# Optimization experiments

Measured on AMD Instinct MI355X. Metric: run time of the kernel, lower is better.

Reference implementation:

```python
import jax, jax.numpy as jnp
import numpy as np

BSZ, SLEN, DIN = 4, 2048, 1024
EMB, HNO = 1024, 16
HSZ = EMB // HNO


def setup_inputs() -> dict:
    key = jax.random.key(0)
    ks = jax.random.split(key, 7)
    s = 1.0 / np.sqrt(DIN)
    return {
        "x": jax.random.normal(ks[0], (BSZ, SLEN, DIN), dtype=jnp.float32),
        "Wq": jax.random.uniform(ks[1], (EMB, DIN), jnp.float32, -s, s),
        "bq": jax.random.uniform(ks[2], (EMB,), jnp.float32, -s, s),
        "Wk": jax.random.uniform(ks[3], (EMB, DIN), jnp.float32, -s, s),
        "bk": jax.random.uniform(ks[4], (EMB,), jnp.float32, -s, s),
        "Wv": jax.random.uniform(ks[5], (EMB, DIN), jnp.float32, -s, s),
        "bv": jax.random.uniform(ks[6], (EMB,), jnp.float32, -s, s),
    }


def reference(x, Wq, bq, Wk, bk, Wv, bv):
    bsz, slen, _ = x.shape
    # QKV projections, split heads: [b, h, s, hd]
    def proj(W, b):
        y = jnp.einsum('bsd,ed->bse', x, W) + b
        return y.reshape(bsz, slen, HNO, HSZ).transpose(0, 2, 1, 3)
    q, k, v = proj(Wq, bq), proj(Wk, bk), proj(Wv, bv)
    # scaled causal attention scores [b, h, s, s]
    scores = jnp.einsum('bhqd,bhkd->bhqk', q, k) / jnp.sqrt(jnp.asarray(HSZ, x.dtype))
    causal = jnp.tril(jnp.ones((slen, slen), dtype=bool))
    scores = jnp.where(causal[None, None], scores, -jnp.inf)
    attn = jax.nn.softmax(scores, axis=-1)
    value = jnp.einsum('bhqk,bhkd->bhqd', attn, v)  # [b, h, s, hd]
    # faithful to source: swap (s, hd) THEN flatten to [b, s, emb]
    value = jnp.swapaxes(value, -2, -1).reshape(bsz, slen, -1)
    return value
```

## Files before the change

### kernel.cpp

```cpp
#include <hip/hip_runtime.h>


#define BSZ 4
#define SLEN 2048
#define DIN 1024
#define EMB 1024
#define HNO 16
#define HSZ 64

typedef unsigned short u16;
typedef __bf16 bf16x8_t __attribute__((ext_vector_type(8)));
typedef float f32x4_t __attribute__((ext_vector_type(4)));

__device__ __forceinline__ u16 f2bf(float f) {
    unsigned u = __float_as_uint(f);
    u += 0x7FFFu + ((u >> 16) & 1u);
    return (u16)(u >> 16);
}

__device__ __forceinline__ float exp2_fast(float x) {
    float r;
    asm("v_exp_f32 %0, %1" : "=v"(r) : "v"(x));
    return r;
}

__device__ __forceinline__ unsigned cvt_pk_bf16(float lo, float hi) {
    unsigned r;
    asm("v_cvt_pk_bf16_f32 %0, %1, %2" : "=v"(r) : "v"(lo), "v"(hi));
    return r;
}

__device__ __forceinline__ void gld16(void* lds, const void* g) {
    __builtin_amdgcn_global_load_lds(
        (const __attribute__((address_space(1))) void*)g,
        (__attribute__((address_space(3))) void*)lds, 16, 0, 0);
}

__global__ __launch_bounds__(256) void cvt_bf16_kernel(
    const float* __restrict__ x,  const float* __restrict__ wq,
    const float* __restrict__ wk, const float* __restrict__ wv,
    u16* __restrict__ xo, u16* __restrict__ wo)
{
    const int y = blockIdx.y;
    const float* src = (y == 0) ? x : (y == 1) ? wq : (y == 2) ? wk : wv;
    u16* dst = (y == 0) ? xo : wo + (size_t)(y - 1) * (EMB * DIN);
    const int n8 = (y == 0) ? (BSZ * SLEN * DIN / 8) : (EMB * DIN / 8);

    for (int i = blockIdx.x * 256 + threadIdx.x; i < n8; i += gridDim.x * 256) {
        float4 a = *reinterpret_cast<const float4*>(src + (size_t)i * 8);
        float4 b = *reinterpret_cast<const float4*>(src + (size_t)i * 8 + 4);
        union { u16 h[8]; uint4 u; } p;
        p.h[0] = f2bf(a.x); p.h[1] = f2bf(a.y); p.h[2] = f2bf(a.z); p.h[3] = f2bf(a.w);
        p.h[4] = f2bf(b.x); p.h[5] = f2bf(b.y); p.h[6] = f2bf(b.z); p.h[7] = f2bf(b.w);
        *reinterpret_cast<uint4*>(dst + (size_t)i * 8) = p.u;
    }
}

__global__ __launch_bounds__(256) void qkv_gemm_kernel(
    const u16* __restrict__ xb, const u16* __restrict__ wb,
    const float* __restrict__ bq, const float* __restrict__ bk,
    const float* __restrict__ bv,
    u16* __restrict__ qo, u16* __restrict__ ko, u16* __restrict__ vo)
{
    __shared__ __attribute__((aligned(16))) u16 As[128][32];
    __shared__ __attribute__((aligned(16))) u16 Bs[128][32];

    const int t    = threadIdx.x;
    const int wid  = t >> 6;
    const int lane = t & 63;
    const int g    = lane >> 4;
    const int r16  = lane & 15;

    const int m0  = blockIdx.x * 128;
    const int n0  = blockIdx.y * 128;
    const int mat = blockIdx.z;

    const u16*   W    = wb + (size_t)mat * (EMB * DIN);
    const float* bias = (mat == 0) ? bq : (mat == 1) ? bk : bv;
    u16*         outp = (mat == 0) ? qo : (mat == 1) ? ko : vo;
    const float  qs   = (mat == 0) ? 0.125f * 1.44269504f : 1.0f;

    const int wm = wid >> 1, wn = wid & 1;

    const int srow = lane >> 2;
    const int scol = (lane & 3) * 8;
    const u16* gA = xb + (size_t)(m0 + wid * 16 + srow) * DIN + scol;
    const u16* gB = W  + (size_t)(n0 + wid * 16 + srow) * DIN + scol;
    u16* lA0 = &As[wid * 16][0];
    u16* lA1 = &As[64 + wid * 16][0];
    u16* lB0 = &Bs[wid * 16][0];
    u16* lB1 = &Bs[64 + wid * 16][0];

    f32x4_t acc[4][4] = {};

    for (int k0 = 0; k0 < DIN; k0 += 32) {
        __syncthreads();
        gld16(lA0, gA + k0);
        gld16(lA1, gA + (size_t)64 * DIN + k0);
        gld16(lB0, gB + k0);
        gld16(lB1, gB + (size_t)64 * DIN + k0);
        __syncthreads();

        bf16x8_t af[4], bfv[4];
#pragma unroll
        for (int i = 0; i < 4; ++i)
            af[i] = *reinterpret_cast<const bf16x8_t*>(&As[wm * 64 + i * 16 + r16][g * 8]);
#pragma unroll
        for (int j = 0; j < 4; ++j)
            bfv[j] = *reinterpret_cast<const bf16x8_t*>(&Bs[wn * 64 + j * 16 + r16][g * 8]);
#pragma unroll
        for (int i = 0; i < 4; ++i)
#pragma unroll
            for (int j = 0; j < 4; ++j)
                acc[i][j] = __builtin_amdgcn_mfma_f32_16x16x32_bf16(af[i], bfv[j], acc[i][j], 0, 0, 0);
    }

#pragma unroll
    for (int j = 0; j < 4; ++j) {
        int e = n0 + wn * 64 + j * 16 + r16;
        float bv_ = bias[e];
        int h = e >> 6, d = e & 63;
#pragma unroll
        for (int i = 0; i < 4; ++i) {
#pragma unroll
            for (int r = 0; r < 4; ++r) {
                int m = m0 + wm * 64 + i * 16 + g * 4 + r;
                int b = m >> 11, s = m & 2047;
                float val = (acc[i][j][r] + bv_) * qs;
                outp[(((size_t)(b * HNO + h)) * SLEN + s) * HSZ + d] = f2bf(val);
            }
        }
    }
}

__global__ __launch_bounds__(512, 6) void attn_kernel(
    const u16* __restrict__ qb, const u16* __restrict__ kb,
    const u16* __restrict__ vb, float* __restrict__ out)
{
    __shared__ __attribute__((aligned(16))) u16 Ks[64][64];
    __shared__ __attribute__((aligned(16))) u16 Vt[64][72];
    __shared__ __attribute__((aligned(16))) u16 P2[8][16][72];

    const int t    = threadIdx.x;
    const int wid  = t >> 6;
    const int lane = t & 63;
    const int g    = lane >> 4;
    const int r16  = lane & 15;

    const int w   = blockIdx.x;
    const int idx = w >> 3;
    const int bh  = (w & 7) * 8 + (idx & 7);
    const int qt  = 15 - (idx >> 3);
    const int q0  = qt * 128;
    const size_t base = (size_t)bh * (SLEN * HSZ);

    const int qi = q0 + wid * 16 + r16;
    bf16x8_t qf0 = *reinterpret_cast<const bf16x8_t*>(&qb[base + (size_t)qi * HSZ + g * 8]);
    bf16x8_t qf1 = *reinterpret_cast<const bf16x8_t*>(&qb[base + (size_t)qi * HSZ + 32 + g * 8]);

    const int krl   = lane >> 3;
    const int kchunk = ((lane & 7) ^ krl) * 8;
    const int krow_g = wid * 8 + krl;
    u16* kdst = &Ks[wid * 8][0];

    const int va  = t & 31;
    const int vc4 = (t >> 5) * 4;

    const int ksl = ((g ^ (r16 & 7)) * 8);

    f32x4_t o[4] = {};
    float mrow = -1e30f, lrow = 0.f;

    const int ntiles = 2 * qt + 2;
    const int qw0 = q0 + wid * 16;
    const int qmax_wave = qw0 + 15;

    uint2 v0 = *reinterpret_cast<const uint2*>(&vb[base + (size_t)(2 * va) * HSZ + vc4]);
    uint2 v1 = *reinterpret_cast<const uint2*>(&vb[base + (size_t)(2 * va + 1) * HSZ + vc4]);

    for (int kt = 0; kt < ntiles; ++kt) {
        const int kv0 = kt * 64;
        __syncthreads();
        gld16(kdst, &kb[base + (size_t)(kv0 + krow_g) * HSZ + kchunk]);
        {
            const unsigned* pa = reinterpret_cast<const unsigned*>(&v0);
            const unsigned* pb = reinterpret_cast<const unsigned*>(&v1);
#pragma unroll
            for (int j2 = 0; j2 < 2; ++j2) {
                unsigned lo = __builtin_amdgcn_perm(pb[j2], pa[j2], 0x05040100u);
                unsigned hi = __builtin_amdgcn_perm(pb[j2], pa[j2], 0x07060302u);
                *reinterpret_cast<unsigned*>(&Vt[vc4 + 2 * j2][2 * va])     = lo;
                *reinterpret_cast<unsigned*>(&Vt[vc4 + 2 * j2 + 1][2 * va]) = hi;
            }
        }
        __syncthreads();

        if (kt + 1 < ntiles) {
            const size_t nb = base + (size_t)(kv0 + 64) * HSZ;
            v0 = *reinterpret_cast<const uint2*>(&vb[nb + (size_t)(2 * va) * HSZ + vc4]);
            v1 = *reinterpret_cast<const uint2*>(&vb[nb + (size_t)(2 * va + 1) * HSZ + vc4]);
        }

        if (kv0 > qmax_wave) continue;

        f32x4_t c_[4];
        __builtin_amdgcn_s_setprio(1);
#pragma unroll
        for (int m = 0; m < 4; ++m) {
            bf16x8_t a0 = *reinterpret_cast<const bf16x8_t*>(&Ks[m * 16 + r16][ksl]);
            bf16x8_t a1 = *reinterpret_cast<const bf16x8_t*>(&Ks[m * 16 + r16][ksl ^ 32]);
            f32x4_t cc = {};
            cc = __builtin_amdgcn_mfma_f32_16x16x32_bf16(a0, qf0, cc, 0, 0, 0);
            cc = __builtin_amdgcn_mfma_f32_16x16x32_bf16(a1, qf1, cc, 0, 0, 0);
            c_[m] = cc;
        }
        __builtin_amdgcn_s_setprio(0);

        float s[16];
        if (kv0 + 63 > qw0) {
#pragma unroll
            for (int m = 0; m < 4; ++m)
#pragma unroll
                for (int r = 0; r < 4; ++r) {
                    int kj = kv0 + m * 16 + g * 4 + r;
                    s[m * 4 + r] = (kj <= qi) ? c_[m][r] : -1e30f;
                }
        } else {
#pragma unroll
            for (int m = 0; m < 4; ++m)
#pragma unroll
                for (int r = 0; r < 4; ++r)
                    s[m * 4 + r] = c_[m][r];
        }
        float x0 = fmaxf(s[0], s[1]),   x1 = fmaxf(s[2], s[3]);
        float x2 = fmaxf(s[4], s[5]),   x3 = fmaxf(s[6], s[7]);
        float x4 = fmaxf(s[8], s[9]),   x5 = fmaxf(s[10], s[11]);
        float x6 = fmaxf(s[12], s[13]), x7 = fmaxf(s[14], s[15]);
        x0 = fmaxf(x0, x1); x2 = fmaxf(x2, x3); x4 = fmaxf(x4, x5); x6 = fmaxf(x6, x7);
        float tmax = fmaxf(fmaxf(x0, x2), fmaxf(x4, x6));
        tmax = fmaxf(tmax, __shfl_xor(tmax, 16));
        tmax = fmaxf(tmax, __shfl_xor(tmax, 32));

        if (!__all(tmax - mrow <= 8.0f)) {
            float mnew  = fmaxf(mrow, tmax);
            float alpha = exp2_fast(mrow - mnew);
#pragma unroll
            for (int j = 0; j < 4; ++j) {
                o[j][0] *= alpha; o[j][1] *= alpha; o[j][2] *= alpha; o[j][3] *= alpha;
            }
            lrow *= alpha;
            mrow = mnew;
        }

#pragma unroll
        for (int i = 0; i < 16; ++i)
            s[i] = exp2_fast(s[i] - mrow);
        float y0 = (s[0] + s[1]) + (s[2] + s[3]);
        float y1 = (s[4] + s[5]) + (s[6] + s[7]);
        float y2 = (s[8] + s[9]) + (s[10] + s[11]);
        float y3 = (s[12] + s[13]) + (s[14] + s[15]);
        float tsum = (y0 + y1) + (y2 + y3);
        tsum += __shfl_xor(tsum, 16);
        tsum += __shfl_xor(tsum, 32);
        lrow += tsum;

#pragma unroll
        for (int m = 0; m < 4; ++m) {
            uint2 pk;
            pk.x = cvt_pk_bf16(s[m * 4 + 0], s[m * 4 + 1]);
            pk.y = cvt_pk_bf16(s[m * 4 + 2], s[m * 4 + 3]);
            *reinterpret_cast<uint2*>(&P2[wid][r16][m * 16 + g * 4]) = pk;
        }

        __builtin_amdgcn_s_setprio(1);
#pragma unroll
        for (int c = 0; c < 2; ++c) {
            bf16x8_t pf = *reinterpret_cast<const bf16x8_t*>(&P2[wid][r16][c * 32 + g * 8]);
#pragma unroll
            for (int j = 0; j < 4; ++j) {
                bf16x8_t vf = *reinterpret_cast<const bf16x8_t*>(&Vt[j * 16 + r16][c * 32 + g * 8]);
                o[j] = __builtin_amdgcn_mfma_f32_16x16x32_bf16(vf, pf, o[j], 0, 0, 0);
            }
        }
        __builtin_amdgcn_s_setprio(0);
    }

    float rinv = 1.0f / lrow;
    const int b = bh >> 4, h = bh & 15;
    float* outb = out + (size_t)b * (SLEN * EMB) + (size_t)h * (HSZ * SLEN);
#pragma unroll
    for (int j = 0; j < 4; ++j) {
#pragma unroll
        for (int r = 0; r < 4; ++r) {
            int d = j * 16 + g * 4 + r;
            outb[(size_t)d * SLEN + qi] = o[j][r] * rinv;
        }
    }
}

extern "C" void kernel_launch(void* const* d_in, const int* in_sizes, int n_in,
                              void* d_out, int out_size, void* d_ws, size_t ws_size,
                              hipStream_t stream) {
    const float* x  = (const float*)d_in[0];
    const float* Wq = (const float*)d_in[1];
    const float* bq = (const float*)d_in[2];
    const float* Wk = (const float*)d_in[3];
    const float* bk = (const float*)d_in[4];
    const float* Wv = (const float*)d_in[5];
    const float* bv = (const float*)d_in[6];
    float* out = (float*)d_out;

    const size_t per = (size_t)BSZ * HNO * SLEN * HSZ;
    u16* qw = (u16*)d_ws;
    u16* kw = qw + per;
    u16* vw = kw + per;

    u16* xb = (u16*)d_out;
    u16* wb = xb + (size_t)BSZ * SLEN * DIN;

    cvt_bf16_kernel<<<dim3(256, 4), 256, 0, stream>>>(x, Wq, Wk, Wv, xb, wb);
    qkv_gemm_kernel<<<dim3(64, 8, 3), 256, 0, stream>>>(xb, wb, bq, bk, bv, qw, kw, vw);
    attn_kernel<<<1024, 512, 0, stream>>>(qw, kw, vw, out);
}
```

Before: 136.3 us.

## Rewrite QKV GEMM as double-buffered 256x192 tile with interleaved async loads

Replaces the 128x128 single-buffered QKV GEMM with a 512-thread, 256x192-tile kernel that treats the three weight matrices as one fused 3072-wide N dimension. It double-buffers LDS with XOR-swizzled layouts, interleaves global-to-LDS stages between MFMA phases, and uses setprio plus sched_barrier to overlap loads with compute. A grid swizzle remaps block indices for L2 locality. This targets the memory stalls and barrier overhead of the old loop, at the cost of much higher register and LDS pressure and fragile hand-tuned vmcnt accounting.

```diff
diff --git a/kernel.cpp b/kernel.cpp
--- a/kernel.cpp
+++ b/kernel.cpp
@@ -56,78 +56,169 @@
     }
 }
 
-__global__ __launch_bounds__(256) void qkv_gemm_kernel(
+#define FENCE() asm volatile("" ::: "memory")
+
+#define RD_A4(mb, kk, buf)                                                     \
+    _Pragma("unroll")                                                          \
+    for (int mm = 0; mm < 4; ++mm)                                             \
+        af[mm][kk] = *reinterpret_cast<const bf16x8_t*>(                       \
+            AsF + (buf) * 16384 + aBase + ((mb) + mm) * 1024 +                 \
+            ((kk) ? (s0 ^ 32) : s0));
+
+#define RD_B3(kk, buf)                                                         \
+    _Pragma("unroll")                                                          \
+    for (int nn = 0; nn < 3; ++nn)                                             \
+        bf[nn][kk] = *reinterpret_cast<const bf16x8_t*>(                       \
+            BsF + (buf) * 12288 + bBase + nn * 1024 +                          \
+            ((kk) ? (s0 ^ 32) : s0));
+
+#define STAGE_A(buf, kt, u)                                                    \
+    gld16(AsF + (buf) * 16384 + (u) * 4096 + t * 8,                            \
+          srcA + (size_t)(u) * 64 * DIN + (kt) * 64)
+
+#define STAGE_B(buf, kt, u)                                                    \
+    gld16(BsF + (buf) * 12288 + (u) * 4096 + t * 8,                            \
+          srcB + (size_t)(u) * 64 * DIN + (kt) * 64)
+
+#define BAR_LGKM()                                                             \
+    __builtin_amdgcn_s_barrier();                                              \
+    asm volatile("s_waitcnt lgkmcnt(0)" ::: "memory");                         \
+    __builtin_amdgcn_sched_barrier(0);                                         \
+    __builtin_amdgcn_s_setprio(1)
+
+#define MFMA12(mb, kk)                                                         \
+    _Pragma("unroll")                                                          \
+    for (int mm = 0; mm < 4; ++mm) {                                           \
+        _Pragma("unroll")                                                      \
+        for (int nn = 0; nn < 3; ++nn)                                         \
+            acc[(mb) + mm][nn] = __builtin_amdgcn_mfma_f32_16x16x32_bf16(      \
+                af[mm][kk], bf[nn][kk], acc[(mb) + mm][nn], 0, 0, 0);          \
+    }
+
+#define MFMA_END()                                                             \
+    __builtin_amdgcn_s_setprio(0);                                             \
+    __builtin_amdgcn_sched_barrier(0)
+
+__global__ __launch_bounds__(512, 2) void qkv_gemm_kernel(
     const u16* __restrict__ xb, const u16* __restrict__ wb,
     const float* __restrict__ bq, const float* __restrict__ bk,
-    const float* __restrict__ bv,
-    u16* __restrict__ qo, u16* __restrict__ ko, u16* __restrict__ vo)
+    const float* __restrict__ bv, u16* __restrict__ qkv)
 {
-    __shared__ __attribute__((aligned(16))) u16 As[128][32];
-    __shared__ __attribute__((aligned(16))) u16 Bs[128][32];
+    __shared__ __attribute__((aligned(16))) u16 AsF[2 * 256 * 64];
+    __shared__ __attribute__((aligned(16))) u16 BsF[2 * 192 * 64];
 
     const int t    = threadIdx.x;
     const int wid  = t >> 6;
     const int lane = t & 63;
     const int g    = lane >> 4;
     const int r16  = lane & 15;
-
-    const int m0  = blockIdx.x * 128;
-    const int n0  = blockIdx.y * 128;
-    const int mat = blockIdx.z;
-
-    const u16*   W    = wb + (size_t)mat * (EMB * DIN);
-    const float* bias = (mat == 0) ? bq : (mat == 1) ? bk : bv;
-    u16*         outp = (mat == 0) ? qo : (mat == 1) ? ko : vo;
-    const float  qs   = (mat == 0) ? 0.125f * 1.44269504f : 1.0f;
-
-    const int wm = wid >> 1, wn = wid & 1;
-
-    const int srow = lane >> 2;
-    const int scol = (lane & 3) * 8;
-    const u16* gA = xb + (size_t)(m0 + wid * 16 + srow) * DIN + scol;
-    const u16* gB = W  + (size_t)(n0 + wid * 16 + srow) * DIN + scol;
-    u16* lA0 = &As[wid * 16][0];
-    u16* lA1 = &As[64 + wid * 16][0];
-    u16* lB0 = &Bs[wid * 16][0];
-    u16* lB1 = &Bs[64 + wid * 16][0];
-
-    f32x4_t acc[4][4] = {};
-
-    for (int k0 = 0; k0 < DIN; k0 += 32) {
-        __syncthreads();
-        gld16(lA0, gA + k0);
-        gld16(lA1, gA + (size_t)64 * DIN + k0);
-        gld16(lB0, gB + k0);
-        gld16(lB1, gB + (size_t)64 * DIN + k0);
-        __syncthreads();
-
-        bf16x8_t af[4], bfv[4];
-#pragma unroll
-        for (int i = 0; i < 4; ++i)
-            af[i] = *reinterpret_cast<const bf16x8_t*>(&As[wm * 64 + i * 16 + r16][g * 8]);
-#pragma unroll
-        for (int j = 0; j < 4; ++j)
-            bfv[j] = *reinterpret_cast<const bf16x8_t*>(&Bs[wn * 64 + j * 16 + r16][g * 8]);
-#pragma unroll
-        for (int i = 0; i < 4; ++i)
-#pragma unroll
-            for (int j = 0; j < 4; ++j)
-                acc[i][j] = __builtin_amdgcn_mfma_f32_16x16x32_bf16(af[i], bfv[j], acc[i][j], 0, 0, 0);
-    }
-
-#pragma unroll
-    for (int j = 0; j < 4; ++j) {
-        int e = n0 + wn * 64 + j * 16 + r16;
-        float bv_ = bias[e];
-        int h = e >> 6, d = e & 63;
-#pragma unroll
-        for (int i = 0; i < 4; ++i) {
+    const int r8   = r16 & 7;
+    const int wm   = wid >> 2;
+    const int wn   = wid & 3;
+
+    const int wg  = blockIdx.x;
+    const int idx = (wg & 7) * 64 + (wg >> 3);
+    const int bx  = idx >> 4;
+    const int byn = idx & 15;
+    const int m0  = bx * 256;
+    const int n0g = byn * 192;
+
+    const int rowoff = t >> 3;
+    const int colswz = ((t & 7) ^ (rowoff & 7)) * 8;
+    const u16* srcA = xb + (size_t)(m0 + rowoff) * DIN + colswz;
+    const u16* srcB = wb + (size_t)(n0g + rowoff) * DIN + colswz;
+
+    const int aBase = (wm * 128 + r16) * 64;
+    const int bBase = (wn * 48 + r16) * 64;
+    const int s0    = (g ^ r8) * 8;
+
+    f32x4_t  acc[8][3] = {};
+    bf16x8_t af[4][2], bf[3][2];
+
+    STAGE_A(0, 0, 0); STAGE_A(0, 0, 1); STAGE_A(0, 0, 2); STAGE_A(0, 0, 3);
+    STAGE_B(0, 0, 0); STAGE_B(0, 0, 1); STAGE_B(0, 0, 2);
+    STAGE_B(1, 1, 0); STAGE_B(1, 1, 1); STAGE_B(1, 1, 2); STAGE_A(1, 1, 0);
+    asm volatile("s_waitcnt vmcnt(4)" ::: "memory");
+    __builtin_amdgcn_s_barrier();
+
+#pragma unroll 1
+    for (int i = 0; i < 8; ++i) {
+        const bool last = (i == 7);
+        const int  tb = 2 * i + 1;
+        const int  ta = 2 * i + 2;
+        const int  tc = 2 * i + 3;
+
+        FENCE();
+        RD_A4(0, 0, 0); RD_B3(0, 0);
+        STAGE_A(1, tb, 2);
+        BAR_LGKM(); MFMA12(0, 0); MFMA_END();
+        __builtin_amdgcn_s_barrier();
+
+        FENCE();
+        RD_A4(0, 1, 0); RD_B3(1, 0);
+        STAGE_A(1, tb, 1); STAGE_A(1, tb, 3);
+        BAR_LGKM(); MFMA12(0, 1); MFMA_END();
+        __builtin_amdgcn_s_barrier();
+
+        FENCE();
+        RD_A4(4, 0, 0);
+        if (!last) { STAGE_B(0, ta, 0); STAGE_B(0, ta, 1); }
+        BAR_LGKM(); MFMA12(4, 0); MFMA_END();
+        __builtin_amdgcn_s_barrier();
+
+        FENCE();
+        RD_A4(4, 1, 0);
+        if (!last) { STAGE_B(0, ta, 2); STAGE_A(0, ta, 0); }
+        BAR_LGKM(); MFMA12(4, 1); MFMA_END();
+        if (!last) asm volatile("s_waitcnt vmcnt(4)" ::: "memory");
+        else       asm volatile("s_waitcnt vmcnt(0)" ::: "memory");
+        __builtin_amdgcn_s_barrier();
+
+        FENCE();
+        RD_A4(0, 0, 1); RD_B3(0, 1);
+        if (!last) STAGE_A(0, ta, 2);
+        BAR_LGKM(); MFMA12(0, 0); MFMA_END();
+        __builtin_amdgcn_s_barrier();
+
+        FENCE();
+        RD_A4(0, 1, 1); RD_B3(1, 1);
+        if (!last) { STAGE_A(0, ta, 1); STAGE_A(0, ta, 3); }
+        BAR_LGKM(); MFMA12(0, 1); MFMA_END();
+        __builtin_amdgcn_s_barrier();
+
+        FENCE();
+        RD_A4(4, 0, 1);
+        if (!last) { STAGE_B(1, tc, 0); STAGE_B(1, tc, 1); }
+        BAR_LGKM(); MFMA12(4, 0); MFMA_END();
+        __builtin_amdgcn_s_barrier();
+
+        FENCE();
+        RD_A4(4, 1, 1);
+        if (!last) { STAGE_B(1, tc, 2); STAGE_A(1, tc, 0); }
+        BAR_LGKM(); MFMA12(4, 1); MFMA_END();
+        if (!last) asm volatile("s_waitcnt vmcnt(4)" ::: "memory");
+        __builtin_amdgcn_s_barrier();
+    }
+
+    const size_t per = (size_t)BSZ * HNO * SLEN * HSZ;
+#pragma unroll
+    for (int nn = 0; nn < 3; ++nn) {
+        const int egl = n0g + wn * 48 + nn * 16 + r16;
+        const int mat = egl >> 10;
+        const int e   = egl & 1023;
+        const float* bp = (mat == 0) ? bq : (mat == 1) ? bk : bv;
+        const float bval = bp[e];
+        const float qsv  = (mat == 0) ? 0.125f * 1.44269504f : 1.0f;
+        const int h = e >> 6, d = e & 63;
+        u16* ob = qkv + (size_t)mat * per + (size_t)h * (SLEN * HSZ) + d;
+#pragma unroll
+        for (int mm = 0; mm < 8; ++mm) {
 #pragma unroll
             for (int r = 0; r < 4; ++r) {
-                int m = m0 + wm * 64 + i * 16 + g * 4 + r;
+                int m = m0 + wm * 128 + mm * 16 + g * 4 + r;
                 int b = m >> 11, s = m & 2047;
-                float val = (acc[i][j][r] + bv_) * qs;
-                outp[(((size_t)(b * HNO + h)) * SLEN + s) * HSZ + d] = f2bf(val);
+                ob[(size_t)b * (HNO * SLEN * HSZ) + (size_t)s * HSZ] =
+                    f2bf((acc[mm][nn][r] + bval) * qsv);
             }
         }
     }
@@ -158,7 +249,7 @@
     bf16x8_t qf0 = *reinterpret_cast<const bf16x8_t*>(&qb[base + (size_t)qi * HSZ + g * 8]);
     bf16x8_t qf1 = *reinterpret_cast<const bf16x8_t*>(&qb[base + (size_t)qi * HSZ + 32 + g * 8]);
 
-    const int krl   = lane >> 3;
+    const int krl    = lane >> 3;
     const int kchunk = ((lane & 7) ^ krl) * 8;
     const int krow_g = wid * 8 + krl;
     u16* kdst = &Ks[wid * 8][0];
@@ -319,6 +410,6 @@
     u16* wb = xb + (size_t)BSZ * SLEN * DIN;
 
     cvt_bf16_kernel<<<dim3(256, 4), 256, 0, stream>>>(x, Wq, Wk, Wv, xb, wb);
-    qkv_gemm_kernel<<<dim3(64, 8, 3), 256, 0, stream>>>(xb, wb, bq, bk, bv, qw, kw, vw);
+    qkv_gemm_kernel<<<512, 512, 0, stream>>>(xb, wb, bq, bk, bv, qw);
     attn_kernel<<<1024, 512, 0, stream>>>(qw, kw, vw, out);
 }
```

Measured after the change: 140.9 us. +3.4%, slower.

## Rework QKV GEMM with BK=64 swizzled LDS, fused QKV N, staged coalesced epilogue

Applied to the files above, without the earlier changes.

The QKV projection GEMM now treats Q, K and V as a single N=3072 problem. It launches a 1D grid whose block-index remap is meant to improve L2 reuse of the x and W tiles. Each iteration loads a K-slice of 64 into XOR-swizzled LDS to avoid bank conflicts and halve the number of barriers. The epilogue stages the bf16 results through shared memory so the head-split output is written as 16-byte coalesced stores instead of scattered 2-byte stores. The larger LDS footprint and the extra epilogue barriers may limit occupancy, which is capped at three blocks per CU by launch bounds.

```diff
diff --git a/kernel.cpp b/kernel.cpp
--- a/kernel.cpp
+++ b/kernel.cpp
@@ -56,79 +56,119 @@
     }
 }
 
-__global__ __launch_bounds__(256) void qkv_gemm_kernel(
+__global__ __launch_bounds__(256, 3) void qkv_gemm_kernel(
     const u16* __restrict__ xb, const u16* __restrict__ wb,
     const float* __restrict__ bq, const float* __restrict__ bk,
-    const float* __restrict__ bv,
-    u16* __restrict__ qo, u16* __restrict__ ko, u16* __restrict__ vo)
+    const float* __restrict__ bv, u16* __restrict__ qkv)
 {
-    __shared__ __attribute__((aligned(16))) u16 As[128][32];
-    __shared__ __attribute__((aligned(16))) u16 Bs[128][32];
+    __shared__ __attribute__((aligned(16))) u16 SH[2 * 128 * 64];
+    u16* AsF = SH;
+    u16* BsF = SH + 128 * 64;
 
     const int t    = threadIdx.x;
     const int wid  = t >> 6;
     const int lane = t & 63;
     const int g    = lane >> 4;
     const int r16  = lane & 15;
-
-    const int m0  = blockIdx.x * 128;
-    const int n0  = blockIdx.y * 128;
-    const int mat = blockIdx.z;
-
-    const u16*   W    = wb + (size_t)mat * (EMB * DIN);
-    const float* bias = (mat == 0) ? bq : (mat == 1) ? bk : bv;
-    u16*         outp = (mat == 0) ? qo : (mat == 1) ? ko : vo;
-    const float  qs   = (mat == 0) ? 0.125f * 1.44269504f : 1.0f;
-
-    const int wm = wid >> 1, wn = wid & 1;
-
-    const int srow = lane >> 2;
-    const int scol = (lane & 3) * 8;
-    const u16* gA = xb + (size_t)(m0 + wid * 16 + srow) * DIN + scol;
-    const u16* gB = W  + (size_t)(n0 + wid * 16 + srow) * DIN + scol;
-    u16* lA0 = &As[wid * 16][0];
-    u16* lA1 = &As[64 + wid * 16][0];
-    u16* lB0 = &Bs[wid * 16][0];
-    u16* lB1 = &Bs[64 + wid * 16][0];
+    const int wm   = wid >> 1, wn = wid & 1;
+
+    const int wg = blockIdx.x;
+    const int x  = wg & 7;
+    const int j  = wg >> 3;
+    const int bx  = (x & 3) * 16 + (j & 15);
+    const int byn = (x >> 2) * 12 + (j >> 4);
+    const int m0  = bx * 128;
+    const int n0g = byn * 128;
+
+    const int rowoff = t >> 3;
+    const int colswz = ((t & 7) ^ (rowoff & 7)) * 8;
+    const u16* srcA = xb + (size_t)(m0 + rowoff) * DIN + colswz;
+    const u16* srcB = wb + (size_t)(n0g + rowoff) * DIN + colswz;
+
+    const int s0 = (g ^ (r16 & 7)) * 8;
 
     f32x4_t acc[4][4] = {};
 
-    for (int k0 = 0; k0 < DIN; k0 += 32) {
-        __syncthreads();
-        gld16(lA0, gA + k0);
-        gld16(lA1, gA + (size_t)64 * DIN + k0);
-        gld16(lB0, gB + k0);
-        gld16(lB1, gB + (size_t)64 * DIN + k0);
+#pragma unroll 1
+    for (int kt = 0; kt < 16; ++kt) {
+        __syncthreads();
+#pragma unroll
+        for (int u = 0; u < 4; ++u) {
+            gld16(AsF + u * 2048 + t * 8,
+                  srcA + (size_t)u * 32 * DIN + kt * 64);
+            gld16(BsF + u * 2048 + t * 8,
+                  srcB + (size_t)u * 32 * DIN + kt * 64);
+        }
         __syncthreads();
 
         bf16x8_t af[4], bfv[4];
 #pragma unroll
-        for (int i = 0; i < 4; ++i)
-            af[i] = *reinterpret_cast<const bf16x8_t*>(&As[wm * 64 + i * 16 + r16][g * 8]);
-#pragma unroll
-        for (int j = 0; j < 4; ++j)
-            bfv[j] = *reinterpret_cast<const bf16x8_t*>(&Bs[wn * 64 + j * 16 + r16][g * 8]);
-#pragma unroll
-        for (int i = 0; i < 4; ++i)
-#pragma unroll
-            for (int j = 0; j < 4; ++j)
-                acc[i][j] = __builtin_amdgcn_mfma_f32_16x16x32_bf16(af[i], bfv[j], acc[i][j], 0, 0, 0);
-    }
-
-#pragma unroll
-    for (int j = 0; j < 4; ++j) {
-        int e = n0 + wn * 64 + j * 16 + r16;
-        float bv_ = bias[e];
-        int h = e >> 6, d = e & 63;
-#pragma unroll
-        for (int i = 0; i < 4; ++i) {
-#pragma unroll
-            for (int r = 0; r < 4; ++r) {
-                int m = m0 + wm * 64 + i * 16 + g * 4 + r;
-                int b = m >> 11, s = m & 2047;
-                float val = (acc[i][j][r] + bv_) * qs;
-                outp[(((size_t)(b * HNO + h)) * SLEN + s) * HSZ + d] = f2bf(val);
+        for (int i2 = 0; i2 < 4; ++i2) {
+            af[i2]  = *reinterpret_cast<const bf16x8_t*>(
+                AsF + (wm * 64 + i2 * 16 + r16) * 64 + s0);
+            bfv[i2] = *reinterpret_cast<const bf16x8_t*>(
+                BsF + (wn * 64 + i2 * 16 + r16) * 64 + s0);
+        }
+#pragma unroll
+        for (int i2 = 0; i2 < 4; ++i2)
+#pragma unroll
+            for (int j2 = 0; j2 < 4; ++j2)
+                acc[i2][j2] = __builtin_amdgcn_mfma_f32_16x16x32_bf16(
+                    af[i2], bfv[j2], acc[i2][j2], 0, 0, 0);
+#pragma unroll
+        for (int i2 = 0; i2 < 4; ++i2) {
+            af[i2]  = *reinterpret_cast<const bf16x8_t*>(
+                AsF + (wm * 64 + i2 * 16 + r16) * 64 + (s0 ^ 32));
+            bfv[i2] = *reinterpret_cast<const bf16x8_t*>(
+                BsF + (wn * 64 + i2 * 16 + r16) * 64 + (s0 ^ 32));
+        }
+#pragma unroll
+        for (int i2 = 0; i2 < 4; ++i2)
+#pragma unroll
+            for (int j2 = 0; j2 < 4; ++j2)
+                acc[i2][j2] = __builtin_amdgcn_mfma_f32_16x16x32_bf16(
+                    af[i2], bfv[j2], acc[i2][j2], 0, 0, 0);
+    }
+
+    const size_t per = (size_t)BSZ * HNO * SLEN * HSZ;
+    u16* lout = SH;
+#pragma unroll
+    for (int h = 0; h < 2; ++h) {
+        __syncthreads();
+        if (wm == h) {
+#pragma unroll
+            for (int j2 = 0; j2 < 4; ++j2) {
+                const int el  = wn * 64 + j2 * 16 + r16;
+                const int egl = n0g + el;
+                const int mat = egl >> 10;
+                const int e   = egl & 1023;
+                const float* bp = (mat == 0) ? bq : (mat == 1) ? bk : bv;
+                const float bval = bp[e];
+                const float qsv  = (mat == 0) ? 0.125f * 1.44269504f : 1.0f;
+#pragma unroll
+                for (int i2 = 0; i2 < 4; ++i2)
+#pragma unroll
+                    for (int r = 0; r < 4; ++r) {
+                        int ml = i2 * 16 + g * 4 + r;
+                        lout[ml * 136 + el] =
+                            f2bf((acc[i2][j2][r] + bval) * qsv);
+                    }
             }
+        }
+        __syncthreads();
+#pragma unroll
+        for (int it = 0; it < 4; ++it) {
+            int cid = it * 256 + t;
+            int row = cid >> 4;
+            int cc  = cid & 15;
+            int egl = n0g + cc * 8;
+            int mat = egl >> 10;
+            int e   = egl & 1023;
+            int m   = m0 + h * 64 + row;
+            int b   = m >> 11, s = m & 2047;
+            uint4 v = *reinterpret_cast<const uint4*>(&lout[row * 136 + cc * 8]);
+            *reinterpret_cast<uint4*>(qkv + (size_t)mat * per +
+                ((((size_t)b * HNO) + (e >> 6)) * SLEN + s) * HSZ + (e & 63)) = v;
         }
     }
 }
@@ -158,7 +198,7 @@
     bf16x8_t qf0 = *reinterpret_cast<const bf16x8_t*>(&qb[base + (size_t)qi * HSZ + g * 8]);
     bf16x8_t qf1 = *reinterpret_cast<const bf16x8_t*>(&qb[base + (size_t)qi * HSZ + 32 + g * 8]);
 
-    const int krl   = lane >> 3;
+    const int krl    = lane >> 3;
     const int kchunk = ((lane & 7) ^ krl) * 8;
     const int krow_g = wid * 8 + krl;
     u16* kdst = &Ks[wid * 8][0];
@@ -245,8 +285,8 @@
             float mnew  = fmaxf(mrow, tmax);
             float alpha = exp2_fast(mrow - mnew);
 #pragma unroll
-            for (int j = 0; j < 4; ++j) {
-                o[j][0] *= alpha; o[j][1] *= alpha; o[j][2] *= alpha; o[j][3] *= alpha;
+            for (int j2 = 0; j2 < 4; ++j2) {
+                o[j2][0] *= alpha; o[j2][1] *= alpha; o[j2][2] *= alpha; o[j2][3] *= alpha;
             }
             lrow *= alpha;
             mrow = mnew;
@@ -277,9 +317,9 @@
         for (int c = 0; c < 2; ++c) {
             bf16x8_t pf = *reinterpret_cast<const bf16x8_t*>(&P2[wid][r16][c * 32 + g * 8]);
 #pragma unroll
-            for (int j = 0; j < 4; ++j) {
-                bf16x8_t vf = *reinterpret_cast<const bf16x8_t*>(&Vt[j * 16 + r16][c * 32 + g * 8]);
-                o[j] = __builtin_amdgcn_mfma_f32_16x16x32_bf16(vf, pf, o[j], 0, 0, 0);
+            for (int j2 = 0; j2 < 4; ++j2) {
+                bf16x8_t vf = *reinterpret_cast<const bf16x8_t*>(&Vt[j2 * 16 + r16][c * 32 + g * 8]);
+                o[j2] = __builtin_amdgcn_mfma_f32_16x16x32_bf16(vf, pf, o[j2], 0, 0, 0);
             }
         }
         __builtin_amdgcn_s_setprio(0);
@@ -289,11 +329,11 @@
     const int b = bh >> 4, h = bh & 15;
     float* outb = out + (size_t)b * (SLEN * EMB) + (size_t)h * (HSZ * SLEN);
 #pragma unroll
-    for (int j = 0; j < 4; ++j) {
+    for (int j2 = 0; j2 < 4; ++j2) {
 #pragma unroll
         for (int r = 0; r < 4; ++r) {
-            int d = j * 16 + g * 4 + r;
-            outb[(size_t)d * SLEN + qi] = o[j][r] * rinv;
+            int d = j2 * 16 + g * 4 + r;
+            outb[(size_t)d * SLEN + qi] = o[j2][r] * rinv;
         }
     }
 }
@@ -319,6 +359,6 @@
     u16* wb = xb + (size_t)BSZ * SLEN * DIN;
 
     cvt_bf16_kernel<<<dim3(256, 4), 256, 0, stream>>>(x, Wq, Wk, Wv, xb, wb);
-    qkv_gemm_kernel<<<dim3(64, 8, 3), 256, 0, stream>>>(xb, wb, bq, bk, bv, qw, kw, vw);
+    qkv_gemm_kernel<<<1536, 256, 0, stream>>>(xb, wb, bq, bk, bv, qw);
     attn_kernel<<<1024, 512, 0, stream>>>(qw, kw, vw, out);
 }
```

Result: faster. 127.8 us (-6.2%).
